# Optimization experiments

Measured on AMD Instinct MI355X. Metric: run time of the kernel, lower is better.

Reference implementation:

```python
import jax, jax.numpy as jnp
import numpy as np

FILTER_P = 0.5
LOG_CLAMP = -100.0  # torch BCELoss clamps log terms at -100


def _zs_substep(img, step):
    """One Zhang-Suen thinning sub-iteration. img: int32 [H, W] in {0,1}.
    skimage.morphology.skeletonize uses Zhang-Suen for 2D inputs."""
    p = jnp.pad(img, 1)
    P2 = p[:-2, 1:-1]; P3 = p[:-2, 2:];  P4 = p[1:-1, 2:];  P5 = p[2:, 2:]
    P6 = p[2:, 1:-1];  P7 = p[2:, :-2];  P8 = p[1:-1, :-2]; P9 = p[:-2, :-2]
    nbrs = jnp.stack([P2, P3, P4, P5, P6, P7, P8, P9, P2])  # cyclic order
    B = nbrs[:8].sum(0)                                      # neighbor count
    A = ((nbrs[:-1] == 0) & (nbrs[1:] == 1)).sum(0)          # 0->1 transitions
    if step == 0:
        c1 = P2 * P4 * P6 == 0
        c2 = P4 * P6 * P8 == 0
    else:
        c1 = P2 * P4 * P8 == 0
        c2 = P2 * P6 * P8 == 0
    remove = (img == 1) & (B >= 2) & (B <= 6) & (A == 1) & c1 & c2
    return img * (1 - remove.astype(img.dtype))


def skeletonize(mask):
    """Zhang-Suen skeletonization. mask: bool [H, W] -> bool [H, W]."""
    img0 = mask.astype(jnp.int32)

    def body(state):
        img, _ = state
        new = _zs_substep(_zs_substep(img, 0), 1)
        return new, jnp.any(new != img)

    img, _ = jax.lax.while_loop(lambda s: s[1], body, (img0, jnp.bool_(True)))
    return img == 1


def setup_inputs() -> dict:
    key = jax.random.key(0)
    k1, k2 = jax.random.split(key)
    B, C, H, W = 8, 1, 512, 512
    pred = jax.random.uniform(k1, (B, C, H, W), dtype=jnp.float32)
    target = jax.random.uniform(k2, (B, C, H, W), dtype=jnp.float32)
    return {"pred": pred, "target": target}


def reference(pred, target):
    # [B, 1, H, W] -> [B, H, W]  (matches pred[i].squeeze(0))
    p2 = pred[:, 0]
    t2 = target[:, 0].astype(pred.dtype)

    gt_bin = t2 > 0.5
    pr_bin = p2 > FILTER_P
    gt_sk = jax.vmap(skeletonize)(gt_bin)
    pr_sk = jax.vmap(skeletonize)(pr_bin)

    # xor(and(gt_sk, pred_bin), gt_sk) == gt_sk & ~pred_bin (and symmetrically)
    positive_sel = gt_sk & (~pr_bin)
    negative_sel = pr_sk & (~gt_bin)
    sel = jax.lax.stop_gradient(positive_sel | negative_sel)

    # BCE with torch-style log clamping, masked mean per sample
    logp = jnp.clip(jnp.log(p2), LOG_CLAMP)
    log1mp = jnp.clip(jnp.log1p(-p2), LOG_CLAMP)
    bce = -(t2 * logp + (1.0 - t2) * log1mp)

    m = sel.astype(pred.dtype)
    cnt = m.sum(axis=(1, 2))                     # [B]
    per = jnp.where(cnt > 0,
                    (bce * m).sum(axis=(1, 2)) / jnp.maximum(cnt, 1.0),
                    0.0)
    total = per.sum() / pred.shape[0]
    return jnp.reshape(total, (1,))
```

## Files before the change

kernel.cpp:

```cpp
#include <hip/hip_runtime.h>
#include <stdint.h>

#define HW 512
#define WPR 8
#define IMG_WORDS (HW * WPR)
#define NIMG 8
#define PIX_PER_IMG (HW * HW)
#define TOTAL_PIX (NIMG * PIX_PER_IMG)
#define MASK_WORDS (TOTAL_PIX / 64)

#define NTASK 16
#define NSTRIP 16
#define SROWS 32
#define GW 16
#define BROWS 64
#define LSTRIDE 65
#define CS 16
#define MAXCHUNK 38

#define CONV_U32 (NTASK * 64)
#define HALO_U64 (NTASK * 15 * 2 * 2 * 128)

#define NBCE (TOTAL_PIX / 2048)

__global__ void pack_kernel(const float* __restrict__ pred,
                            const float* __restrict__ target,
                            uint64_t* __restrict__ gt_bin,
                            uint64_t* __restrict__ pr_bin,
                            uint32_t* __restrict__ conv) {
    int idx = blockIdx.x * 256 + threadIdx.x;
    if (blockIdx.x < 4) {
        int z = blockIdx.x * 256 + threadIdx.x;
        conv[z] = 0u;
    }
    float p = pred[idx];
    float t = target[idx];
    uint64_t bp = __ballot(p > 0.5f);
    uint64_t bt = __ballot(t > 0.5f);
    if ((threadIdx.x & 63) == 0) {
        int w = idx >> 6;
        pr_bin[w] = bp;
        gt_bin[w] = bt;
    }
}

__device__ __forceinline__ uint64_t zs_win2(int step, const uint64_t (&Uw)[4],
                                            const uint64_t (&Cw)[4],
                                            const uint64_t (&Dw)[4],
                                            uint64_t (&NEW)[2]) {
    uint64_t changed = 0;
#pragma unroll
    for (int j = 1; j <= 2; ++j) {
        uint64_t P2 = Uw[j];
        uint64_t P6 = Dw[j];
        uint64_t P4 = (Cw[j] >> 1) | (Cw[j + 1] << 63);
        uint64_t P8 = (Cw[j] << 1) | (Cw[j - 1] >> 63);
        uint64_t P3 = (Uw[j] >> 1) | (Uw[j + 1] << 63);
        uint64_t P9 = (Uw[j] << 1) | (Uw[j - 1] >> 63);
        uint64_t P5 = (Dw[j] >> 1) | (Dw[j + 1] << 63);
        uint64_t P7 = (Dw[j] << 1) | (Dw[j - 1] >> 63);

        uint64_t s1 = P2 ^ P3, sum1 = s1 ^ P4, car1 = (P2 & P3) | (P4 & s1);
        uint64_t s2 = P5 ^ P6, sum2 = s2 ^ P7, car2 = (P5 & P6) | (P7 & s2);
        uint64_t s3 = sum1 ^ sum2, sum3 = s3 ^ P8, car3 = (sum1 & sum2) | (P8 & s3);
        uint64_t b0 = sum3 ^ P9, car4 = sum3 & P9;
        uint64_t s5 = car1 ^ car2, sum5 = s5 ^ car3, car5 = (car1 & car2) | (car3 & s5);
        uint64_t b1 = sum5 ^ car4, car6 = sum5 & car4;
        uint64_t b2 = car5 ^ car6, b3 = car5 & car6;
        uint64_t ge2 = b1 | b2 | b3;
        uint64_t le6 = ~(b3 | (b0 & b1 & b2));
        uint64_t condB = ge2 & le6;

        uint64_t t0 = ~P2 & P3, t1 = ~P3 & P4, t2 = ~P4 & P5, t3 = ~P5 & P6;
        uint64_t t4 = ~P6 & P7, t5 = ~P7 & P8, t6 = ~P8 & P9, t7 = ~P9 & P2;
        uint64_t a01 = t0 | t1, a23 = t2 | t3, a45 = t4 | t5, a67 = t6 | t7;
        uint64_t m2 = (t0 & t1) | (t2 & t3) | (t4 & t5) | (t6 & t7);
        uint64_t a0123 = a01 | a23, a4567 = a45 | a67;
        m2 |= (a01 & a23) | (a45 & a67);
        m2 |= a0123 & a4567;
        uint64_t condA = (a0123 | a4567) & ~m2;

        uint64_t c1, c2;
        if (step == 0) {
            uint64_t q = P4 & P6;
            c1 = ~(q & P2);
            c2 = ~(q & P8);
        } else {
            uint64_t q = P2 & P8;
            c1 = ~(q & P4);
            c2 = ~(q & P6);
        }
        uint64_t rem = Cw[j] & condB & condA & c1 & c2;
        NEW[j - 1] = Cw[j] & ~rem;
        changed |= rem;
    }
    return changed;
}

__global__ __launch_bounds__(256) void skel_kernel(const uint64_t* __restrict__ bin,
                                                   uint64_t* __restrict__ sk,
                                                   uint64_t* __restrict__ halo,
                                                   uint32_t* __restrict__ conv) {
    __shared__ uint64_t sbuf[2][WPR * LSTRIDE];
    __shared__ int s_any4[4];
    __shared__ int s_dec;
    const int tid = threadIdx.x;
    const int task = blockIdx.x & (NTASK - 1);
    const int strip = blockIdx.x >> 4;
    const int rl = tid >> 2;
    const int wb = (tid & 3) * 2;
    const int gr0 = strip * SROWS - GW;
    const uint64_t* src = bin + (size_t)task * IMG_WORDS;
    uint64_t* dst = sk + (size_t)task * IMG_WORDS;

    uint64_t C[2];
    {
        int gr = gr0 + rl;
        bool in = (gr >= 0) && (gr < HW);
        C[0] = in ? src[gr * WPR + wb] : 0ull;
        C[1] = in ? src[gr * WPR + wb + 1] : 0ull;
        sbuf[0][wb * LSTRIDE + rl] = C[0];
        sbuf[0][(wb + 1) * LSTRIDE + rl] = C[1];
    }
    __syncthreads();

    int cb = 0;
    const bool owned = (rl >= GW) && (rl < GW + SROWS);
    for (int chunk = 0; chunk < MAXCHUNK; ++chunk) {
        uint32_t tailch = 0;
        for (int ss = 0; ss < CS; ++ss) {
            const uint64_t* cur = sbuf[cb];
            uint64_t* nxt = sbuf[cb ^ 1];
            uint64_t Uw[4], Dw[4], Cw[4], NEW[2];
#pragma unroll
            for (int j = 0; j < 4; ++j) {
                int gw = wb - 1 + j;
                bool v = (gw >= 0) && (gw < 8);
                Uw[j] = (v && rl > 0)          ? cur[gw * LSTRIDE + rl - 1] : 0ull;
                Dw[j] = (v && rl < BROWS - 1)  ? cur[gw * LSTRIDE + rl + 1] : 0ull;
            }
            Cw[0] = (wb > 0) ? cur[(wb - 1) * LSTRIDE + rl] : 0ull;
            Cw[3] = (wb < 6) ? cur[(wb + 2) * LSTRIDE + rl] : 0ull;
            Cw[1] = C[0];
            Cw[2] = C[1];
            uint64_t ch = zs_win2(ss & 1, Uw, Cw, Dw, NEW);
            if (ss >= CS - 2 && owned && ch) tailch = 1;
            nxt[wb * LSTRIDE + rl] = NEW[0];
            nxt[(wb + 1) * LSTRIDE + rl] = NEW[1];
            C[0] = NEW[0];
            C[1] = NEW[1];
            cb ^= 1;
            __syncthreads();
        }

        const int par = chunk & 1;
        if (strip > 0 && rl >= GW && rl < 2 * GW) {
            uint64_t* hp = halo + ((((size_t)task * 15 + (strip - 1)) * 2 + 0) * 2 + par) * 128
                                + (rl - GW) * 8 + wb;
            __hip_atomic_store(hp, C[0], __ATOMIC_RELAXED, __HIP_MEMORY_SCOPE_AGENT);
            __hip_atomic_store(hp + 1, C[1], __ATOMIC_RELAXED, __HIP_MEMORY_SCOPE_AGENT);
            asm volatile("s_waitcnt vmcnt(0)" ::: "memory");
        }
        if (strip < NSTRIP - 1 && rl >= 32 && rl < 48) {
            uint64_t* hp = halo + ((((size_t)task * 15 + strip) * 2 + 1) * 2 + par) * 128
                                + (rl - 32) * 8 + wb;
            __hip_atomic_store(hp, C[0], __ATOMIC_RELAXED, __HIP_MEMORY_SCOPE_AGENT);
            __hip_atomic_store(hp + 1, C[1], __ATOMIC_RELAXED, __HIP_MEMORY_SCOPE_AGENT);
            asm volatile("s_waitcnt vmcnt(0)" ::: "memory");
        }
        int wa = __any((int)tailch);
        if ((tid & 63) == 0) s_any4[tid >> 6] = wa;
        __syncthreads();
        if (tid == 0) {
            uint32_t add = 256u + ((s_any4[0] | s_any4[1] | s_any4[2] | s_any4[3]) ? 1u : 0u);
            uint32_t* cp = &conv[task * 64 + chunk];
            uint32_t v = __hip_atomic_fetch_add(cp, add, __ATOMIC_RELEASE,
                                                __HIP_MEMORY_SCOPE_AGENT) + add;
            while ((v >> 8) < (uint32_t)NSTRIP)
                v = __hip_atomic_load(cp, __ATOMIC_ACQUIRE, __HIP_MEMORY_SCOPE_AGENT);
            s_dec = ((v & 0xffu) != 0u) ? 1 : 0;
        }
        __syncthreads();
        if (!s_dec) break;

        if (strip > 0 && rl < GW) {
            const uint64_t* hp = halo + ((((size_t)task * 15 + (strip - 1)) * 2 + 1) * 2 + par) * 128
                                      + rl * 8 + wb;
            C[0] = __hip_atomic_load(hp, __ATOMIC_RELAXED, __HIP_MEMORY_SCOPE_AGENT);
            C[1] = __hip_atomic_load(hp + 1, __ATOMIC_RELAXED, __HIP_MEMORY_SCOPE_AGENT);
            sbuf[cb][wb * LSTRIDE + rl] = C[0];
            sbuf[cb][(wb + 1) * LSTRIDE + rl] = C[1];
        }
        if (strip < NSTRIP - 1 && rl >= 48) {
            const uint64_t* hp = halo + ((((size_t)task * 15 + strip) * 2 + 0) * 2 + par) * 128
                                      + (rl - 48) * 8 + wb;
            C[0] = __hip_atomic_load(hp, __ATOMIC_RELAXED, __HIP_MEMORY_SCOPE_AGENT);
            C[1] = __hip_atomic_load(hp + 1, __ATOMIC_RELAXED, __HIP_MEMORY_SCOPE_AGENT);
            sbuf[cb][wb * LSTRIDE + rl] = C[0];
            sbuf[cb][(wb + 1) * LSTRIDE + rl] = C[1];
        }
        __syncthreads();
    }

    if (owned) {
        int gr = gr0 + rl;
        dst[gr * WPR + wb] = C[0];
        dst[gr * WPR + wb + 1] = C[1];
    }
}

__global__ __launch_bounds__(256) void bce_kernel(
        const float4* __restrict__ pred4, const float4* __restrict__ tgt4,
        const uint64_t* __restrict__ gt_bin, const uint64_t* __restrict__ pr_bin,
        const uint64_t* __restrict__ gt_sk, const uint64_t* __restrict__ pr_sk,
        float* __restrict__ psum, int* __restrict__ pcnt) {
    int tg = blockIdx.x * 256 + threadIdx.x;
    int w = tg >> 3;
    uint64_t sel = (gt_sk[w] & ~pr_bin[w]) | (pr_sk[w] & ~gt_bin[w]);
    uint32_t bits = (uint32_t)(sel >> ((tg & 7) * 8)) & 0xffu;
    float4 pa = pred4[2 * tg], pb = pred4[2 * tg + 1];
    float4 ta = tgt4[2 * tg], tb = tgt4[2 * tg + 1];
    float p[8] = {pa.x, pa.y, pa.z, pa.w, pb.x, pb.y, pb.z, pb.w};
    float t[8] = {ta.x, ta.y, ta.z, ta.w, tb.x, tb.y, tb.z, tb.w};
    float lsum = 0.0f;
    int lcnt = 0;
#pragma unroll
    for (int j = 0; j < 8; ++j) {
        float lp = fmaxf(logf(p[j]), -100.0f);
        float l1 = fmaxf(log1pf(-p[j]), -100.0f);
        float b = -(t[j] * lp + (1.0f - t[j]) * l1);
        uint32_t m = (bits >> j) & 1u;
        lsum = fmaf((float)m, b, lsum);
        lcnt += (int)m;
    }
#pragma unroll
    for (int off = 32; off > 0; off >>= 1) {
        lsum += __shfl_down(lsum, off, 64);
        lcnt += __shfl_down(lcnt, off, 64);
    }
    __shared__ float sred[4];
    __shared__ int cred[4];
    int wave = threadIdx.x >> 6, lane = threadIdx.x & 63;
    if (lane == 0) { sred[wave] = lsum; cred[wave] = lcnt; }
    __syncthreads();
    if (threadIdx.x == 0) {
        psum[blockIdx.x] = sred[0] + sred[1] + sred[2] + sred[3];
        pcnt[blockIdx.x] = cred[0] + cred[1] + cred[2] + cred[3];
    }
}

__global__ __launch_bounds__(1024) void final_kernel(const float* __restrict__ psum,
                                                     const int* __restrict__ pcnt,
                                                     float* __restrict__ out) {
    int t = threadIdx.x;
    float s = psum[t];
    int c = pcnt[t];
#pragma unroll
    for (int off = 32; off > 0; off >>= 1) {
        s += __shfl_down(s, off, 64);
        c += __shfl_down(c, off, 64);
    }
    __shared__ float ss[16];
    __shared__ int sc[16];
    int w = t >> 6;
    if ((t & 63) == 0) { ss[w] = s; sc[w] = c; }
    __syncthreads();
    if (t == 0) {
        float tot = 0.0f;
#pragma unroll
        for (int i = 0; i < NIMG; ++i) {
            float sv = ss[2 * i] + ss[2 * i + 1];
            int cv = sc[2 * i] + sc[2 * i + 1];
            tot += (cv > 0) ? sv / (float)cv : 0.0f;
        }
        out[0] = tot * (1.0f / NIMG);
    }
}

extern "C" void kernel_launch(void* const* d_in, const int* in_sizes, int n_in,
                              void* d_out, int out_size, void* d_ws, size_t ws_size,
                              hipStream_t stream) {
    const float* pred = (const float*)d_in[0];
    const float* target = (const float*)d_in[1];
    uint64_t* ws = (uint64_t*)d_ws;
    uint64_t* gt_bin = ws;
    uint64_t* pr_bin = ws + MASK_WORDS;
    uint64_t* gt_sk  = ws + 2 * MASK_WORDS;
    uint64_t* pr_sk  = ws + 3 * MASK_WORDS;
    uint64_t* halo   = ws + 4 * MASK_WORDS;
    uint32_t* conv   = (uint32_t*)(ws + 4 * MASK_WORDS + HALO_U64);
    float* psum      = (float*)(conv + CONV_U32);
    int* pcnt        = (int*)(psum + NBCE);

    pack_kernel<<<TOTAL_PIX / 256, 256, 0, stream>>>(pred, target, gt_bin, pr_bin, conv);
    skel_kernel<<<NTASK * NSTRIP, 256, 0, stream>>>(gt_bin, gt_sk, halo, conv);
    bce_kernel<<<NBCE, 256, 0, stream>>>((const float4*)pred, (const float4*)target,
                                         gt_bin, pr_bin, gt_sk, pr_sk, psum, pcnt);
    final_kernel<<<1, 1024, 0, stream>>>(psum, pcnt, (float*)d_out);
}
```

Before: 95.48 us.

## Fuse binarization into skeleton kernel and use one word per thread

```diff
diff --git a/kernel.cpp b/kernel.cpp
--- a/kernel.cpp
+++ b/kernel.cpp
@@ -14,7 +14,7 @@
 #define SROWS 32
 #define GW 16
 #define BROWS 64
-#define LSTRIDE 65
+#define RSTRIDE 9
 #define CS 16
 #define MAXCHUNK 38
 
@@ -23,106 +23,88 @@
 
 #define NBCE (TOTAL_PIX / 2048)
 
-__global__ void pack_kernel(const float* __restrict__ pred,
-                            const float* __restrict__ target,
-                            uint64_t* __restrict__ gt_bin,
-                            uint64_t* __restrict__ pr_bin,
-                            uint32_t* __restrict__ conv) {
-    int idx = blockIdx.x * 256 + threadIdx.x;
-    if (blockIdx.x < 4) {
-        int z = blockIdx.x * 256 + threadIdx.x;
-        conv[z] = 0u;
-    }
-    float p = pred[idx];
-    float t = target[idx];
-    uint64_t bp = __ballot(p > 0.5f);
-    uint64_t bt = __ballot(t > 0.5f);
-    if ((threadIdx.x & 63) == 0) {
-        int w = idx >> 6;
-        pr_bin[w] = bp;
-        gt_bin[w] = bt;
-    }
-}
-
-__device__ __forceinline__ uint64_t zs_win2(int step, const uint64_t (&Uw)[4],
-                                            const uint64_t (&Cw)[4],
-                                            const uint64_t (&Dw)[4],
-                                            uint64_t (&NEW)[2]) {
-    uint64_t changed = 0;
-#pragma unroll
-    for (int j = 1; j <= 2; ++j) {
-        uint64_t P2 = Uw[j];
-        uint64_t P6 = Dw[j];
-        uint64_t P4 = (Cw[j] >> 1) | (Cw[j + 1] << 63);
-        uint64_t P8 = (Cw[j] << 1) | (Cw[j - 1] >> 63);
-        uint64_t P3 = (Uw[j] >> 1) | (Uw[j + 1] << 63);
-        uint64_t P9 = (Uw[j] << 1) | (Uw[j - 1] >> 63);
-        uint64_t P5 = (Dw[j] >> 1) | (Dw[j + 1] << 63);
-        uint64_t P7 = (Dw[j] << 1) | (Dw[j - 1] >> 63);
-
-        uint64_t s1 = P2 ^ P3, sum1 = s1 ^ P4, car1 = (P2 & P3) | (P4 & s1);
-        uint64_t s2 = P5 ^ P6, sum2 = s2 ^ P7, car2 = (P5 & P6) | (P7 & s2);
-        uint64_t s3 = sum1 ^ sum2, sum3 = s3 ^ P8, car3 = (sum1 & sum2) | (P8 & s3);
-        uint64_t b0 = sum3 ^ P9, car4 = sum3 & P9;
-        uint64_t s5 = car1 ^ car2, sum5 = s5 ^ car3, car5 = (car1 & car2) | (car3 & s5);
-        uint64_t b1 = sum5 ^ car4, car6 = sum5 & car4;
-        uint64_t b2 = car5 ^ car6, b3 = car5 & car6;
-        uint64_t ge2 = b1 | b2 | b3;
-        uint64_t le6 = ~(b3 | (b0 & b1 & b2));
-        uint64_t condB = ge2 & le6;
-
-        uint64_t t0 = ~P2 & P3, t1 = ~P3 & P4, t2 = ~P4 & P5, t3 = ~P5 & P6;
-        uint64_t t4 = ~P6 & P7, t5 = ~P7 & P8, t6 = ~P8 & P9, t7 = ~P9 & P2;
-        uint64_t a01 = t0 | t1, a23 = t2 | t3, a45 = t4 | t5, a67 = t6 | t7;
-        uint64_t m2 = (t0 & t1) | (t2 & t3) | (t4 & t5) | (t6 & t7);
-        uint64_t a0123 = a01 | a23, a4567 = a45 | a67;
-        m2 |= (a01 & a23) | (a45 & a67);
-        m2 |= a0123 & a4567;
-        uint64_t condA = (a0123 | a4567) & ~m2;
-
-        uint64_t c1, c2;
-        if (step == 0) {
-            uint64_t q = P4 & P6;
-            c1 = ~(q & P2);
-            c2 = ~(q & P8);
-        } else {
-            uint64_t q = P2 & P8;
-            c1 = ~(q & P4);
-            c2 = ~(q & P6);
-        }
-        uint64_t rem = Cw[j] & condB & condA & c1 & c2;
-        NEW[j - 1] = Cw[j] & ~rem;
-        changed |= rem;
-    }
-    return changed;
-}
-
-__global__ __launch_bounds__(256) void skel_kernel(const uint64_t* __restrict__ bin,
+__global__ __launch_bounds__(256) void init_kernel(uint32_t* __restrict__ conv) {
+#pragma unroll
+    for (int k = 0; k < 4; ++k) conv[threadIdx.x + k * 256] = 0u;
+}
+
+__device__ __forceinline__ uint64_t zs1(int step, const uint64_t (&Uw)[3],
+                                        const uint64_t (&Cw)[3],
+                                        const uint64_t (&Dw)[3],
+                                        uint64_t& NEW) {
+    uint64_t P2 = Uw[1];
+    uint64_t P6 = Dw[1];
+    uint64_t P4 = (Cw[1] >> 1) | (Cw[2] << 63);
+    uint64_t P8 = (Cw[1] << 1) | (Cw[0] >> 63);
+    uint64_t P3 = (Uw[1] >> 1) | (Uw[2] << 63);
+    uint64_t P9 = (Uw[1] << 1) | (Uw[0] >> 63);
+    uint64_t P5 = (Dw[1] >> 1) | (Dw[2] << 63);
+    uint64_t P7 = (Dw[1] << 1) | (Dw[0] >> 63);
+
+    uint64_t s1 = P2 ^ P3, sum1 = s1 ^ P4, car1 = (P2 & P3) | (P4 & s1);
+    uint64_t s2 = P5 ^ P6, sum2 = s2 ^ P7, car2 = (P5 & P6) | (P7 & s2);
+    uint64_t s3 = sum1 ^ sum2, sum3 = s3 ^ P8, car3 = (sum1 & sum2) | (P8 & s3);
+    uint64_t b0 = sum3 ^ P9, car4 = sum3 & P9;
+    uint64_t s5 = car1 ^ car2, sum5 = s5 ^ car3, car5 = (car1 & car2) | (car3 & s5);
+    uint64_t b1 = sum5 ^ car4, car6 = sum5 & car4;
+    uint64_t b2 = car5 ^ car6, b3 = car5 & car6;
+    uint64_t ge2 = b1 | b2 | b3;
+    uint64_t le6 = ~(b3 | (b0 & b1 & b2));
+    uint64_t condB = ge2 & le6;
+
+    uint64_t t0 = ~P2 & P3, t1 = ~P3 & P4, t2 = ~P4 & P5, t3 = ~P5 & P6;
+    uint64_t t4 = ~P6 & P7, t5 = ~P7 & P8, t6 = ~P8 & P9, t7 = ~P9 & P2;
+    uint64_t a01 = t0 | t1, a23 = t2 | t3, a45 = t4 | t5, a67 = t6 | t7;
+    uint64_t m2 = (t0 & t1) | (t2 & t3) | (t4 & t5) | (t6 & t7);
+    uint64_t a0123 = a01 | a23, a4567 = a45 | a67;
+    m2 |= (a01 & a23) | (a45 & a67);
+    m2 |= a0123 & a4567;
+    uint64_t condA = (a0123 | a4567) & ~m2;
+
+    uint64_t c1, c2;
+    if (step == 0) {
+        uint64_t q = P4 & P6;
+        c1 = ~(q & P2);
+        c2 = ~(q & P8);
+    } else {
+        uint64_t q = P2 & P8;
+        c1 = ~(q & P4);
+        c2 = ~(q & P6);
+    }
+    uint64_t rem = Cw[1] & condB & condA & c1 & c2;
+    NEW = Cw[1] & ~rem;
+    return rem;
+}
+
+__global__ __launch_bounds__(512) void skel_kernel(const float* __restrict__ pred,
+                                                   const float* __restrict__ target,
                                                    uint64_t* __restrict__ sk,
                                                    uint64_t* __restrict__ halo,
                                                    uint32_t* __restrict__ conv) {
-    __shared__ uint64_t sbuf[2][WPR * LSTRIDE];
-    __shared__ int s_any4[4];
+    __shared__ uint64_t sbuf[2][BROWS * RSTRIDE];
+    __shared__ int s_any8[8];
     __shared__ int s_dec;
     const int tid = threadIdx.x;
     const int task = blockIdx.x & (NTASK - 1);
     const int strip = blockIdx.x >> 4;
-    const int rl = tid >> 2;
-    const int wb = (tid & 3) * 2;
+    const int rl = tid >> 3;
+    const int wq = tid & 7;
+    const int lane = tid & 63;
+    const int wave = tid >> 6;
     const int gr0 = strip * SROWS - GW;
-    const uint64_t* src = bin + (size_t)task * IMG_WORDS;
+    const float* srcf = (task < 8 ? target : pred) + (size_t)(task & 7) * PIX_PER_IMG;
     uint64_t* dst = sk + (size_t)task * IMG_WORDS;
 
-    uint64_t C[2];
-    {
-        int gr = gr0 + rl;
-        bool in = (gr >= 0) && (gr < HW);
-        C[0] = in ? src[gr * WPR + wb] : 0ull;
-        C[1] = in ? src[gr * WPR + wb + 1] : 0ull;
-        sbuf[0][wb * LSTRIDE + rl] = C[0];
-        sbuf[0][(wb + 1) * LSTRIDE + rl] = C[1];
+    for (int m = 0; m < 64; ++m) {
+        int k = wave * 64 + m;
+        int r = k >> 3, w = k & 7;
+        int gr = gr0 + r;
+        float f = (gr >= 0 && gr < HW) ? srcf[gr * HW + w * 64 + lane] : 0.0f;
+        uint64_t bits = __ballot(f > 0.5f);
+        if (lane == 0) sbuf[0][r * RSTRIDE + w] = bits;
     }
     __syncthreads();
+    uint64_t C = sbuf[0][rl * RSTRIDE + wq];
 
     int cb = 0;
     const bool owned = (rl >= GW) && (rl < GW + SROWS);
@@ -131,24 +113,21 @@
         for (int ss = 0; ss < CS; ++ss) {
             const uint64_t* cur = sbuf[cb];
             uint64_t* nxt = sbuf[cb ^ 1];
-            uint64_t Uw[4], Dw[4], Cw[4], NEW[2];
-#pragma unroll
-            for (int j = 0; j < 4; ++j) {
-                int gw = wb - 1 + j;
+            uint64_t Uw[3], Cw[3], Dw[3], NEW;
+#pragma unroll
+            for (int j = 0; j < 3; ++j) {
+                int gw = wq - 1 + j;
                 bool v = (gw >= 0) && (gw < 8);
-                Uw[j] = (v && rl > 0)          ? cur[gw * LSTRIDE + rl - 1] : 0ull;
-                Dw[j] = (v && rl < BROWS - 1)  ? cur[gw * LSTRIDE + rl + 1] : 0ull;
+                Uw[j] = (v && rl > 0)          ? cur[(rl - 1) * RSTRIDE + gw] : 0ull;
+                Dw[j] = (v && rl < BROWS - 1)  ? cur[(rl + 1) * RSTRIDE + gw] : 0ull;
             }
-            Cw[0] = (wb > 0) ? cur[(wb - 1) * LSTRIDE + rl] : 0ull;
-            Cw[3] = (wb < 6) ? cur[(wb + 2) * LSTRIDE + rl] : 0ull;
-            Cw[1] = C[0];
-            Cw[2] = C[1];
-            uint64_t ch = zs_win2(ss & 1, Uw, Cw, Dw, NEW);
+            Cw[0] = (wq > 0) ? cur[rl * RSTRIDE + wq - 1] : 0ull;
+            Cw[2] = (wq < 7) ? cur[rl * RSTRIDE + wq + 1] : 0ull;
+            Cw[1] = C;
+            uint64_t ch = zs1(ss & 1, Uw, Cw, Dw, NEW);
             if (ss >= CS - 2 && owned && ch) tailch = 1;
-            nxt[wb * LSTRIDE + rl] = NEW[0];
-            nxt[(wb + 1) * LSTRIDE + rl] = NEW[1];
-            C[0] = NEW[0];
-            C[1] = NEW[1];
+            nxt[rl * RSTRIDE + wq] = NEW;
+            C = NEW;
             cb ^= 1;
             __syncthreads();
         }
@@ -156,23 +135,23 @@
         const int par = chunk & 1;
         if (strip > 0 && rl >= GW && rl < 2 * GW) {
             uint64_t* hp = halo + ((((size_t)task * 15 + (strip - 1)) * 2 + 0) * 2 + par) * 128
-                                + (rl - GW) * 8 + wb;
-            __hip_atomic_store(hp, C[0], __ATOMIC_RELAXED, __HIP_MEMORY_SCOPE_AGENT);
-            __hip_atomic_store(hp + 1, C[1], __ATOMIC_RELAXED, __HIP_MEMORY_SCOPE_AGENT);
+                                + (rl - GW) * 8 + wq;
+            __hip_atomic_store(hp, C, __ATOMIC_RELAXED, __HIP_MEMORY_SCOPE_AGENT);
             asm volatile("s_waitcnt vmcnt(0)" ::: "memory");
         }
         if (strip < NSTRIP - 1 && rl >= 32 && rl < 48) {
             uint64_t* hp = halo + ((((size_t)task * 15 + strip) * 2 + 1) * 2 + par) * 128
-                                + (rl - 32) * 8 + wb;
-            __hip_atomic_store(hp, C[0], __ATOMIC_RELAXED, __HIP_MEMORY_SCOPE_AGENT);
-            __hip_atomic_store(hp + 1, C[1], __ATOMIC_RELAXED, __HIP_MEMORY_SCOPE_AGENT);
+                                + (rl - 32) * 8 + wq;
+            __hip_atomic_store(hp, C, __ATOMIC_RELAXED, __HIP_MEMORY_SCOPE_AGENT);
             asm volatile("s_waitcnt vmcnt(0)" ::: "memory");
         }
         int wa = __any((int)tailch);
-        if ((tid & 63) == 0) s_any4[tid >> 6] = wa;
+        if (lane == 0) s_any8[wave] = wa;
         __syncthreads();
         if (tid == 0) {
-            uint32_t add = 256u + ((s_any4[0] | s_any4[1] | s_any4[2] | s_any4[3]) ? 1u : 0u);
+            int any = s_any8[0] | s_any8[1] | s_any8[2] | s_any8[3]
+                    | s_any8[4] | s_any8[5] | s_any8[6] | s_any8[7];
+            uint32_t add = 256u + (any ? 1u : 0u);
             uint32_t* cp = &conv[task * 64 + chunk];
             uint32_t v = __hip_atomic_fetch_add(cp, add, __ATOMIC_RELEASE,
                                                 __HIP_MEMORY_SCOPE_AGENT) + add;
@@ -185,39 +164,34 @@
 
         if (strip > 0 && rl < GW) {
             const uint64_t* hp = halo + ((((size_t)task * 15 + (strip - 1)) * 2 + 1) * 2 + par) * 128
-                                      + rl * 8 + wb;
-            C[0] = __hip_atomic_load(hp, __ATOMIC_RELAXED, __HIP_MEMORY_SCOPE_AGENT);
-            C[1] = __hip_atomic_load(hp + 1, __ATOMIC_RELAXED, __HIP_MEMORY_SCOPE_AGENT);
-            sbuf[cb][wb * LSTRIDE + rl] = C[0];
-            sbuf[cb][(wb + 1) * LSTRIDE + rl] = C[1];
+                                      + rl * 8 + wq;
+            C = __hip_atomic_load(hp, __ATOMIC_RELAXED, __HIP_MEMORY_SCOPE_AGENT);
+            sbuf[cb][rl * RSTRIDE + wq] = C;
         }
         if (strip < NSTRIP - 1 && rl >= 48) {
             const uint64_t* hp = halo + ((((size_t)task * 15 + strip) * 2 + 0) * 2 + par) * 128
-                                      + (rl - 48) * 8 + wb;
-            C[0] = __hip_atomic_load(hp, __ATOMIC_RELAXED, __HIP_MEMORY_SCOPE_AGENT);
-            C[1] = __hip_atomic_load(hp + 1, __ATOMIC_RELAXED, __HIP_MEMORY_SCOPE_AGENT);
-            sbuf[cb][wb * LSTRIDE + rl] = C[0];
-            sbuf[cb][(wb + 1) * LSTRIDE + rl] = C[1];
+                                      + (rl - 48) * 8 + wq;
+            C = __hip_atomic_load(hp, __ATOMIC_RELAXED, __HIP_MEMORY_SCOPE_AGENT);
+            sbuf[cb][rl * RSTRIDE + wq] = C;
         }
         __syncthreads();
     }
 
     if (owned) {
         int gr = gr0 + rl;
-        dst[gr * WPR + wb] = C[0];
-        dst[gr * WPR + wb + 1] = C[1];
+        dst[gr * WPR + wq] = C;
     }
 }
 
 __global__ __launch_bounds__(256) void bce_kernel(
         const float4* __restrict__ pred4, const float4* __restrict__ tgt4,
-        const uint64_t* __restrict__ gt_bin, const uint64_t* __restrict__ pr_bin,
         const uint64_t* __restrict__ gt_sk, const uint64_t* __restrict__ pr_sk,
         float* __restrict__ psum, int* __restrict__ pcnt) {
     int tg = blockIdx.x * 256 + threadIdx.x;
     int w = tg >> 3;
-    uint64_t sel = (gt_sk[w] & ~pr_bin[w]) | (pr_sk[w] & ~gt_bin[w]);
-    uint32_t bits = (uint32_t)(sel >> ((tg & 7) * 8)) & 0xffu;
+    int sh = (tg & 7) * 8;
+    uint32_t gbits = (uint32_t)(gt_sk[w] >> sh) & 0xffu;
+    uint32_t pbits = (uint32_t)(pr_sk[w] >> sh) & 0xffu;
     float4 pa = pred4[2 * tg], pb = pred4[2 * tg + 1];
     float4 ta = tgt4[2 * tg], tb = tgt4[2 * tg + 1];
     float p[8] = {pa.x, pa.y, pa.z, pa.w, pb.x, pb.y, pb.z, pb.w};
@@ -229,7 +203,10 @@
         float lp = fmaxf(logf(p[j]), -100.0f);
         float l1 = fmaxf(log1pf(-p[j]), -100.0f);
         float b = -(t[j] * lp + (1.0f - t[j]) * l1);
-        uint32_t m = (bits >> j) & 1u;
+        uint32_t prb = (p[j] > 0.5f) ? 1u : 0u;
+        uint32_t gtb = (t[j] > 0.5f) ? 1u : 0u;
+        uint32_t m = (((gbits >> j) & 1u) & (prb ^ 1u))
+                   | (((pbits >> j) & 1u) & (gtb ^ 1u));
         lsum = fmaf((float)m, b, lsum);
         lcnt += (int)m;
     }
@@ -283,18 +260,17 @@
     const float* pred = (const float*)d_in[0];
     const float* target = (const float*)d_in[1];
     uint64_t* ws = (uint64_t*)d_ws;
-    uint64_t* gt_bin = ws;
-    uint64_t* pr_bin = ws + MASK_WORDS;
-    uint64_t* gt_sk  = ws + 2 * MASK_WORDS;
-    uint64_t* pr_sk  = ws + 3 * MASK_WORDS;
-    uint64_t* halo   = ws + 4 * MASK_WORDS;
-    uint32_t* conv   = (uint32_t*)(ws + 4 * MASK_WORDS + HALO_U64);
-    float* psum      = (float*)(conv + CONV_U32);
-    int* pcnt        = (int*)(psum + NBCE);
-
-    pack_kernel<<<TOTAL_PIX / 256, 256, 0, stream>>>(pred, target, gt_bin, pr_bin, conv);
-    skel_kernel<<<NTASK * NSTRIP, 256, 0, stream>>>(gt_bin, gt_sk, halo, conv);
+    uint64_t* sk    = ws;
+    uint64_t* gt_sk = sk;
+    uint64_t* pr_sk = sk + MASK_WORDS;
+    uint64_t* halo  = ws + 2 * MASK_WORDS;
+    uint32_t* conv  = (uint32_t*)(halo + HALO_U64);
+    float* psum     = (float*)(conv + CONV_U32);
+    int* pcnt       = (int*)(psum + NBCE);
+
+    init_kernel<<<1, 256, 0, stream>>>(conv);
+    skel_kernel<<<NTASK * NSTRIP, 512, 0, stream>>>(pred, target, sk, halo, conv);
     bce_kernel<<<NBCE, 256, 0, stream>>>((const float4*)pred, (const float4*)target,
-                                         gt_bin, pr_bin, gt_sk, pr_sk, psum, pcnt);
+                                         gt_sk, pr_sk, psum, pcnt);
     final_kernel<<<1, 1024, 0, stream>>>(psum, pcnt, (float*)d_out);
 }
```

New measurement: 111.0 us. +16.3%, slower.
